# Kernel optimization log

Hardware: AMD Instinct MI355X
Metric: run time of the kernel (lower is better)

The kernel has to match this reference:

```python
import jax, jax.numpy as jnp
import numpy as np

B, T, D, H = 32, 4096, 768, 1024
RHOS = np.linspace(0.1, 0.9, 5)
TAU = 1.0
EPS = 1e-5


def entmax15(x):
    # exact 1.5-entmax along last axis (Peters et al. 2019)
    x = x / 2.0
    x_srt = jnp.flip(jnp.sort(x, axis=-1), axis=-1)  # descending
    n = x.shape[-1]
    rho = jnp.arange(1, n + 1, dtype=x.dtype)
    mean = jnp.cumsum(x_srt, axis=-1) / rho
    mean_sq = jnp.cumsum(x_srt * x_srt, axis=-1) / rho
    ss = rho * (mean_sq - mean * mean)
    delta = (1.0 - ss) / rho
    tau = mean - jnp.sqrt(jnp.clip(delta, 0.0))
    support = jnp.sum(tau <= x_srt, axis=-1, keepdims=True)
    tau_star = jnp.take_along_axis(tau, support - 1, axis=-1)
    return jnp.clip(x - tau_star, 0.0) ** 2


def setup_inputs() -> dict:
    key = jax.random.key(0)
    ks = jax.random.split(key, 8)
    embeddings = jax.random.normal(ks[0], (B, T, D), dtype=jnp.float32)
    ids = jax.random.randint(ks[1], (B, T), 0, 32000)
    lengths = jax.random.randint(ks[2], (B,), T // 4, T + 1)
    attn = (jnp.arange(T)[None, :] < lengths[:, None]).astype(jnp.float32)
    ln_g = jnp.ones((D,), jnp.float32)
    ln_b = jnp.zeros((D,), jnp.float32)
    W1 = 0.02 * jax.random.normal(ks[3], (D, H), dtype=jnp.float32)
    b1 = jnp.zeros((H,), jnp.float32)
    W2 = 0.02 * jax.random.normal(ks[4], (H, 1), dtype=jnp.float32)
    b2 = jnp.zeros((1,), jnp.float32)
    return {"embeddings": embeddings, "attn": attn, "ln_g": ln_g, "ln_b": ln_b,
            "W1": W1, "b1": b1, "W2": W2, "b2": b2, "ids": ids}


def reference(embeddings, attn, ln_g, ln_b, W1, b1, W2, b2, ids):
    emb = embeddings * attn[..., None]                      # [B,T,D]
    mu = jnp.mean(emb, axis=-1, keepdims=True)
    var = jnp.mean((emb - mu) ** 2, axis=-1, keepdims=True)
    xn = (emb - mu) / jnp.sqrt(var + EPS) * ln_g + ln_b
    h1 = jax.nn.gelu(xn @ W1 + b1, approximate=False)       # torch F.gelu (erf)
    scores = (h1 @ W2 + b2)[..., 0]                         # [B,T]
    scores = jnp.where(attn == 0, -1e9, scores)
    z = entmax15(scores / TAU) * attn                       # [B,T]
    sorted_idx = jnp.argsort(-z, axis=-1)                   # descending
    inv_rank = jnp.argsort(sorted_idx, axis=-1)             # rank of each position
    t_eff = jnp.sum(attn, axis=-1)                          # [B]
    rhos = jnp.asarray(RHOS, dtype=z.dtype)                 # [R]
    k = jnp.maximum(1, jnp.floor(rhos[:, None] * t_eff[None, :])).astype(jnp.int32)  # [R,B]
    h = (inv_rank[None] < k[:, :, None]).astype(z.dtype) * attn[None]  # [R,B,T]
    g = jax.lax.stop_gradient(h - z[None]) + z[None]        # straight-through
    return jnp.concatenate([z[None], g], axis=0)            # [1+R, B, T]
```

## Files before the change

### kernel.cpp

```cpp
#include <hip/hip_runtime.h>
#include <math.h>

#define Bc 32
#define Tc 4096
#define Dc 768
#define Hc 1024
#define BTc (Bc*Tc)
#define PLANE 786432

typedef __bf16 bf16x8 __attribute__((ext_vector_type(8)));
typedef float f32x16 __attribute__((ext_vector_type(16)));

__device__ __forceinline__ float gelu_erf(float x) {
  return 0.5f * x * (1.0f + erff(x * 0.70710678118654752440f));
}
__device__ __forceinline__ unsigned bf16rne(float x) {
  unsigned u = __float_as_uint(x);
  return (u + 0x7FFFu + ((u >> 16) & 1u)) >> 16;
}
__device__ __forceinline__ void split3(float x, unsigned& h, unsigned& m, unsigned& l) {
  h = bf16rne(x);
  float r1 = x - __uint_as_float(h << 16);
  m = bf16rne(r1);
  float r2 = r1 - __uint_as_float(m << 16);
  l = bf16rne(r2);
}
__device__ __forceinline__ unsigned f2o(float f) {
  unsigned b = __float_as_uint(f);
  return (b & 0x80000000u) ? ~b : (b | 0x80000000u);
}
__device__ __forceinline__ float o2f(unsigned o) {
  unsigned b = (o & 0x80000000u) ? (o & 0x7FFFFFFFu) : ~o;
  return __uint_as_float(b);
}

struct Bfrag { bf16x8 h[4], m[4], l[4]; };

__device__ __forceinline__ void loadB(const ushort* __restrict__ bp0, Bfrag& B) {
  #pragma unroll
  for (int nt = 0; nt < 4; nt++) {
    const ushort* bp = bp0 + nt * 256;
    B.h[nt] = *(const bf16x8*)(bp);
    B.m[nt] = *(const bf16x8*)(bp + PLANE);
    B.l[nt] = *(const bf16x8*)(bp + 2 * PLANE);
  }
}

__device__ __forceinline__ void mfma6(bf16x8 a0, bf16x8 a1, bf16x8 a2,
                                      const Bfrag& B, f32x16* acc) {
  #pragma unroll
  for (int nt = 0; nt < 4; nt++)
    acc[nt] = __builtin_amdgcn_mfma_f32_32x32x16_bf16(a0, B.h[nt], acc[nt], 0, 0, 0);
  #pragma unroll
  for (int nt = 0; nt < 4; nt++)
    acc[nt] = __builtin_amdgcn_mfma_f32_32x32x16_bf16(a0, B.m[nt], acc[nt], 0, 0, 0);
  #pragma unroll
  for (int nt = 0; nt < 4; nt++)
    acc[nt] = __builtin_amdgcn_mfma_f32_32x32x16_bf16(a1, B.h[nt], acc[nt], 0, 0, 0);
  #pragma unroll
  for (int nt = 0; nt < 4; nt++)
    acc[nt] = __builtin_amdgcn_mfma_f32_32x32x16_bf16(a1, B.m[nt], acc[nt], 0, 0, 0);
  #pragma unroll
  for (int nt = 0; nt < 4; nt++)
    acc[nt] = __builtin_amdgcn_mfma_f32_32x32x16_bf16(a0, B.l[nt], acc[nt], 0, 0, 0);
  #pragma unroll
  for (int nt = 0; nt < 4; nt++)
    acc[nt] = __builtin_amdgcn_mfma_f32_32x32x16_bf16(a2, B.h[nt], acc[nt], 0, 0, 0);
}

__global__ __launch_bounds__(256) void w1_split_k(
    const float* __restrict__ W1, ushort* __restrict__ w1s) {
  int id = blockIdx.x * 256 + threadIdx.x;
  int n = id & 1023, kg = id >> 10;
  unsigned hs[8], ms[8], ls[8];
  #pragma unroll
  for (int j = 0; j < 8; j++) {
    float x = W1[(size_t)(kg * 8 + j) * Hc + n];
    split3(x, hs[j], ms[j], ls[j]);
  }
  size_t o = ((size_t)kg * 1024 + n) * 8;
  int4 ph, pm, pl;
  ph.x = (int)(hs[0] | (hs[1] << 16)); ph.y = (int)(hs[2] | (hs[3] << 16));
  ph.z = (int)(hs[4] | (hs[5] << 16)); ph.w = (int)(hs[6] | (hs[7] << 16));
  pm.x = (int)(ms[0] | (ms[1] << 16)); pm.y = (int)(ms[2] | (ms[3] << 16));
  pm.z = (int)(ms[4] | (ms[5] << 16)); pm.w = (int)(ms[6] | (ms[7] << 16));
  pl.x = (int)(ls[0] | (ls[1] << 16)); pl.y = (int)(ls[2] | (ls[3] << 16));
  pl.z = (int)(ls[4] | (ls[5] << 16)); pl.w = (int)(ls[6] | (ls[7] << 16));
  *(int4*)(w1s + o)             = ph;
  *(int4*)(w1s + o + PLANE)     = pm;
  *(int4*)(w1s + o + 2 * PLANE) = pl;
}

__global__ __launch_bounds__(256) void ln_stats_k(
    const float* __restrict__ emb, const float* __restrict__ attn,
    float* __restrict__ mu, float* __restrict__ rstd) {
  int row = blockIdx.x * 4 + (threadIdx.x >> 6);
  int lane = threadIdx.x & 63;
  float a = attn[row];
  const float4* e = (const float4*)(emb + (size_t)row * Dc);
  float4 v0 = e[lane], v1 = e[lane + 64], v2 = e[lane + 128];
  float x[12] = {v0.x*a, v0.y*a, v0.z*a, v0.w*a,
                 v1.x*a, v1.y*a, v1.z*a, v1.w*a,
                 v2.x*a, v2.y*a, v2.z*a, v2.w*a};
  float s = 0.f;
  #pragma unroll
  for (int i = 0; i < 12; i++) s += x[i];
  #pragma unroll
  for (int o = 32; o; o >>= 1) s += __shfl_xor(s, o);
  float m = s / 768.0f;
  float q = 0.f;
  #pragma unroll
  for (int i = 0; i < 12; i++) { float d = x[i] - m; q += d * d; }
  #pragma unroll
  for (int o = 32; o; o >>= 1) q += __shfl_xor(q, o);
  float var = q / 768.0f;
  if (lane == 0) { mu[row] = m; rstd[row] = 1.0f / sqrtf(var + 1e-5f); }
}

__global__ __launch_bounds__(256, 2) void gemm_scores_mfma8(
    const float* __restrict__ emb, const float* __restrict__ attn,
    const float* __restrict__ ln_g, const float* __restrict__ ln_b,
    const ushort* __restrict__ w1s, const float* __restrict__ b1,
    const float* __restrict__ W2, const float* __restrict__ b2,
    const float* __restrict__ mu, const float* __restrict__ rstd,
    float* __restrict__ spart) {
  __shared__ int4 Abuf[2][3][4][64];
  __shared__ float gls[768], bls[768];
  __shared__ float red[4][64];
  const int id = blockIdx.x;
  const int xcd = id & 7;
  const int y = xcd & 1;
  const int xg = (id >> 3) * 4 + (xcd >> 1);
  const int base = xg * 64;
  if (attn[base] == 0.0f) return;
  const int hbase = y * 512;
  const int t = threadIdx.x;
  const int lane = t & 63;
  const int lrow = lane & 31;
  const int lkg = lane >> 5;
  const int w = t >> 6;

  if (t < 192) {
    *(float4*)&gls[t * 4] = *(const float4*)&ln_g[t * 4];
    *(float4*)&bls[t * 4] = *(const float4*)&ln_b[t * 4];
  }
  const int srow = t & 63;
  const int skg = t >> 6;
  const int skoff = skg * 8;
  const float la  = attn[base + srow];
  const float lmu = mu[base + srow];
  const float lrs = rstd[base + srow];
  const float* erow = emb + (size_t)(base + srow) * Dc + skoff;

  f32x16 acc[8];
  #pragma unroll
  for (int nt = 0; nt < 8; nt++)
    #pragma unroll
    for (int r = 0; r < 16; r++) acc[nt][r] = 0.f;

  __syncthreads();
  {
    float4 e0 = *(const float4*)(erow);
    float4 e1 = *(const float4*)(erow + 4);
    float4 g0 = *(const float4*)&gls[skoff];
    float4 g1 = *(const float4*)&gls[skoff + 4];
    float4 q0 = *(const float4*)&bls[skoff];
    float4 q1 = *(const float4*)&bls[skoff + 4];
    float xs[8] = {e0.x,e0.y,e0.z,e0.w,e1.x,e1.y,e1.z,e1.w};
    float gs[8] = {g0.x,g0.y,g0.z,g0.w,g1.x,g1.y,g1.z,g1.w};
    float bs[8] = {q0.x,q0.y,q0.z,q0.w,q1.x,q1.y,q1.z,q1.w};
    unsigned hh[8], hm[8], hl[8];
    #pragma unroll
    for (int e = 0; e < 8; e++) {
      float xn = (xs[e] * la - lmu) * lrs * gs[e] + bs[e];
      split3(xn, hh[e], hm[e], hl[e]);
    }
    int4 ph, pm, pl;
    ph.x = (int)(hh[0] | (hh[1] << 16)); ph.y = (int)(hh[2] | (hh[3] << 16));
    ph.z = (int)(hh[4] | (hh[5] << 16)); ph.w = (int)(hh[6] | (hh[7] << 16));
    pm.x = (int)(hm[0] | (hm[1] << 16)); pm.y = (int)(hm[2] | (hm[3] << 16));
    pm.z = (int)(hm[4] | (hm[5] << 16)); pm.w = (int)(hm[6] | (hm[7] << 16));
    pl.x = (int)(hl[0] | (hl[1] << 16)); pl.y = (int)(hl[2] | (hl[3] << 16));
    pl.z = (int)(hl[4] | (hl[5] << 16)); pl.w = (int)(hl[6] | (hl[7] << 16));
    Abuf[0][0][skg][srow] = ph;
    Abuf[0][1][skg][srow] = pm;
    Abuf[0][2][skg][srow] = pl;
  }
  __syncthreads();

  const ushort* wbase = w1s + ((size_t)hbase + w * 128 + lrow) * 8;

  #pragma unroll 1
  for (int i = 0; i < 24; i++) {
    const int p = i & 1;
    const bool more = (i < 23);
    #pragma unroll
    for (int kh = 0; kh < 2; kh++) {
      const int kg = kh * 2 + lkg;
      bf16x8 a00 = *(const bf16x8*)&Abuf[p][0][kg][lrow];
      bf16x8 a01 = *(const bf16x8*)&Abuf[p][1][kg][lrow];
      bf16x8 a02 = *(const bf16x8*)&Abuf[p][2][kg][lrow];
      bf16x8 a10 = *(const bf16x8*)&Abuf[p][0][kg][32 + lrow];
      bf16x8 a11 = *(const bf16x8*)&Abuf[p][1][kg][32 + lrow];
      bf16x8 a12 = *(const bf16x8*)&Abuf[p][2][kg][32 + lrow];
      Bfrag B;
      loadB(wbase + (size_t)(i * 4 + kg) * 8192, B);
      mfma6(a00, a01, a02, B, acc);
      mfma6(a10, a11, a12, B, acc + 4);
    }
    if (more) {
      const float* ep = erow + (i + 1) * 32;
      const int koff = (i + 1) * 32 + skoff;
      float4 e0 = *(const float4*)(ep);
      float4 e1 = *(const float4*)(ep + 4);
      float4 g0 = *(const float4*)&gls[koff];
      float4 g1 = *(const float4*)&gls[koff + 4];
      float4 q0 = *(const float4*)&bls[koff];
      float4 q1 = *(const float4*)&bls[koff + 4];
      float xs[8] = {e0.x,e0.y,e0.z,e0.w,e1.x,e1.y,e1.z,e1.w};
      float gs[8] = {g0.x,g0.y,g0.z,g0.w,g1.x,g1.y,g1.z,g1.w};
      float bs[8] = {q0.x,q0.y,q0.z,q0.w,q1.x,q1.y,q1.z,q1.w};
      unsigned hh[8], hm[8], hl[8];
      #pragma unroll
      for (int e = 0; e < 8; e++) {
        float xn = (xs[e] * la - lmu) * lrs * gs[e] + bs[e];
        split3(xn, hh[e], hm[e], hl[e]);
      }
      int4 ph, pm, pl;
      ph.x = (int)(hh[0] | (hh[1] << 16)); ph.y = (int)(hh[2] | (hh[3] << 16));
      ph.z = (int)(hh[4] | (hh[5] << 16)); ph.w = (int)(hh[6] | (hh[7] << 16));
      pm.x = (int)(hm[0] | (hm[1] << 16)); pm.y = (int)(hm[2] | (hm[3] << 16));
      pm.z = (int)(hm[4] | (hm[5] << 16)); pm.w = (int)(hm[6] | (hm[7] << 16));
      pl.x = (int)(hl[0] | (hl[1] << 16)); pl.y = (int)(hl[2] | (hl[3] << 16));
      pl.z = (int)(hl[4] | (hl[5] << 16)); pl.w = (int)(hl[6] | (hl[7] << 16));
      Abuf[p ^ 1][0][skg][srow] = ph;
      Abuf[p ^ 1][1][skg][srow] = pm;
      Abuf[p ^ 1][2][skg][srow] = pl;
    }
    __syncthreads();
  }

  #pragma unroll
  for (int rt = 0; rt < 2; rt++) {
    float sacc[16];
    #pragma unroll
    for (int r = 0; r < 16; r++) sacc[r] = 0.f;
    #pragma unroll
    for (int nt = 0; nt < 4; nt++) {
      const int col = hbase + w * 128 + nt * 32 + lrow;
      const float b1v = b1[col];
      const float w2v = W2[col];
      #pragma unroll
      for (int r = 0; r < 16; r++)
        sacc[r] += gelu_erf(acc[rt * 4 + nt][r] + b1v) * w2v;
    }
    #pragma unroll
    for (int r = 0; r < 16; r++) {
      float v = sacc[r];
      v += __shfl_xor(v, 1);  v += __shfl_xor(v, 2);  v += __shfl_xor(v, 4);
      v += __shfl_xor(v, 8);  v += __shfl_xor(v, 16);
      if (lrow == 0) {
        int row = rt * 32 + (r & 3) + 8 * (r >> 2) + 4 * lkg;
        red[w][row] = v;
      }
    }
  }
  __syncthreads();
  if (t < 64) {
    float v = red[0][t] + red[1][t] + red[2][t] + red[3][t];
    if (y == 0) v += b2[0];
    spart[y * BTc + base + t] = v;
  }
}

__global__ __launch_bounds__(256) void entmax_rank_k(
    const float* __restrict__ sp0, const float* __restrict__ sp1,
    const float* __restrict__ attn, float* __restrict__ out) {
  const int N = 4096;
  __shared__ unsigned long long keys[4096];
  __shared__ double tsum[256], tsq[256];
  __shared__ int tcnt[256];
  __shared__ float sred[4];
  __shared__ double sh_tau;
  __shared__ int sh_S, sh_m, sh_k[5];
  const int b = blockIdx.x;
  const int t = threadIdx.x;
  const float* srow0 = sp0 + b * N;
  const float* srow1 = sp1 + b * N;
  const float* arow = attn + b * N;
  float teff_l = 0.f;
  for (int i = t; i < N; i += 256) {
    float a = arow[i];
    float s = srow0[i] + srow1[i];
    float xe = (a == 0.f) ? -1e9f : s;
    teff_l += a;
    keys[i] = ((unsigned long long)f2o(xe) << 32) |
              (unsigned long long)(0xFFFFFFFFu - (unsigned)i);
  }
  #pragma unroll
  for (int o = 32; o; o >>= 1) teff_l += __shfl_xor(teff_l, o);
  if ((t & 63) == 0) sred[t >> 6] = teff_l;
  __syncthreads();
  if (t == 0) {
    float te = sred[0] + sred[1] + sred[2] + sred[3];
    const float rh[5] = {0.1f, 0.3f, 0.5f, 0.7f, 0.9f};
    for (int r = 0; r < 5; r++) {
      int ki = (int)floorf(rh[r] * te);
      sh_k[r] = ki < 1 ? 1 : ki;
    }
  }
  for (int kk = 2; kk <= N; kk <<= 1) {
    for (int j = kk >> 1; j > 0; j >>= 1) {
      __syncthreads();
      for (int idx = t; idx < N / 2; idx += 256) {
        int i = 2 * idx - (idx & (j - 1));
        int l = i | j;
        unsigned long long A = keys[i], Bv = keys[l];
        bool up = ((i & kk) == 0);
        if (up ? (A < Bv) : (A > Bv)) { keys[i] = Bv; keys[l] = A; }
      }
    }
  }
  __syncthreads();
  const int base = t * 16;
  {
    double ls = 0, lq = 0;
    for (int ii = 0; ii < 16; ii++) {
      double x = 0.5 * (double)o2f((unsigned)(keys[base + ii] >> 32));
      ls += x; lq += x * x;
    }
    tsum[t] = ls; tsq[t] = lq;
  }
  __syncthreads();
  if (t == 0) {
    double rs = 0, rq = 0;
    for (int i = 0; i < 256; i++) {
      double a = tsum[i], c = tsq[i];
      tsum[i] = rs; tsq[i] = rq; rs += a; rq += c;
    }
  }
  __syncthreads();
  {
    double cs = tsum[t], cq = tsq[t];
    int lc = 0;
    for (int ii = 0; ii < 16; ii++) {
      double x = 0.5 * (double)o2f((unsigned)(keys[base + ii] >> 32));
      cs += x; cq += x * x;
      double rho = (double)(base + ii + 1);
      double mean = cs / rho, msq = cq / rho;
      double ss = rho * (msq - mean * mean);
      double delta = (1.0 - ss) / rho;
      double dl = delta > 0.0 ? delta : 0.0;
      double tau = mean - sqrt(dl);
      if (tau <= x) lc++;
    }
    tcnt[t] = lc;
  }
  __syncthreads();
  if (t == 0) {
    int r = 0;
    for (int i = 0; i < 256; i++) { int c = tcnt[i]; tcnt[i] = r; r += c; }
    sh_S = r;
  }
  __syncthreads();
  {
    int jstar = sh_S - 1;
    if (jstar >= base && jstar < base + 16) {
      double cs = tsum[t], cq = tsq[t], tau = 0.0;
      for (int ii = 0; ii <= jstar - base; ii++) {
        double x = 0.5 * (double)o2f((unsigned)(keys[base + ii] >> 32));
        cs += x; cq += x * x;
        double rho = (double)(base + ii + 1);
        double mean = cs / rho, msq = cq / rho;
        double ss = rho * (msq - mean * mean);
        double delta = (1.0 - ss) / rho;
        double dl = delta > 0.0 ? delta : 0.0;
        tau = mean - sqrt(dl);
      }
      sh_tau = tau;
    }
  }
  __syncthreads();
  const double tau = sh_tau;
  float ps[16], pa[16];
  {
    int lf = 0;
    for (int ii = 0; ii < 16; ii++) {
      int p = base + ii;
      ps[ii] = srow0[p] + srow1[p]; pa[ii] = arow[p];
      double d = 0.5 * (double)ps[ii] - tau;
      if (pa[ii] != 0.f && d > 0.0) lf++;
    }
    tcnt[t] = lf;
  }
  __syncthreads();
  if (t == 0) {
    int r = 0;
    for (int i = 0; i < 256; i++) { int c = tcnt[i]; tcnt[i] = r; r += c; }
    sh_m = r;
  }
  __syncthreads();
  const int m = sh_m;
  const int k0_ = sh_k[0], k1_ = sh_k[1], k2_ = sh_k[2], k3_ = sh_k[3], k4_ = sh_k[4];
  {
    int cex = tcnt[t];
    for (int ii = 0; ii < 16; ii++) {
      int p = base + ii;
      double d = 0.5 * (double)ps[ii] - tau;
      bool av = (pa[ii] != 0.f);
      bool sup = av && (d > 0.0);
      out[b * N + p] = sup ? (float)(d * d) : 0.0f;
      if (!sup) {
        int rank = m + p - cex;
        out[1 * BTc + b * N + p] = (av && rank < k0_) ? 1.f : 0.f;
        out[2 * BTc + b * N + p] = (av && rank < k1_) ? 1.f : 0.f;
        out[3 * BTc + b * N + p] = (av && rank < k2_) ? 1.f : 0.f;
        out[4 * BTc + b * N + p] = (av && rank < k3_) ? 1.f : 0.f;
        out[5 * BTc + b * N + p] = (av && rank < k4_) ? 1.f : 0.f;
      } else {
        cex++;
      }
    }
  }
  for (int r = t; r < m; r += 256) {
    int i = (int)(0xFFFFFFFFu - (unsigned)(keys[r] & 0xFFFFFFFFull));
    out[1 * BTc + b * N + i] = (r < k0_) ? 1.f : 0.f;
    out[2 * BTc + b * N + i] = (r < k1_) ? 1.f : 0.f;
    out[3 * BTc + b * N + i] = (r < k2_) ? 1.f : 0.f;
    out[4 * BTc + b * N + i] = (r < k3_) ? 1.f : 0.f;
    out[5 * BTc + b * N + i] = (r < k4_) ? 1.f : 0.f;
  }
}

extern "C" void kernel_launch(void* const* d_in, const int* in_sizes, int n_in,
                              void* d_out, int out_size, void* d_ws, size_t ws_size,
                              hipStream_t stream) {
  (void)in_sizes; (void)n_in; (void)out_size; (void)ws_size;
  const float* emb  = (const float*)d_in[0];
  const float* attn = (const float*)d_in[1];
  const float* ln_g = (const float*)d_in[2];
  const float* ln_b = (const float*)d_in[3];
  const float* W1   = (const float*)d_in[4];
  const float* b1   = (const float*)d_in[5];
  const float* W2   = (const float*)d_in[6];
  const float* b2   = (const float*)d_in[7];
  float* out = (float*)d_out;
  float* wsf = (float*)d_ws;
  float* mu     = wsf;
  float* rstd   = wsf + BTc;
  float* spart  = wsf + 2 * BTc;
  ushort* w1s   = (ushort*)(wsf + 4 * BTc);

  w1_split_k<<<384, 256, 0, stream>>>(W1, w1s);
  ln_stats_k<<<BTc / 4, 256, 0, stream>>>(emb, attn, mu, rstd);
  gemm_scores_mfma8<<<4096, 256, 0, stream>>>(
      emb, attn, ln_g, ln_b, w1s, b1, W2, b2, mu, rstd, spart);
  entmax_rank_k<<<Bc, 256, 0, stream>>>(spart, spart + BTc, attn, out);
}
```

Measured before the change: 980.9 us.

## Stage W1 and embedding tiles into LDS via async global_load_lds double buffering

```diff
diff --git a/kernel.cpp b/kernel.cpp
--- a/kernel.cpp
+++ b/kernel.cpp
@@ -11,6 +11,19 @@
 typedef __bf16 bf16x8 __attribute__((ext_vector_type(8)));
 typedef float f32x16 __attribute__((ext_vector_type(16)));
 
+__device__ __forceinline__ void dma16(const void* g, void* l) {
+  __builtin_amdgcn_global_load_lds(
+      (const __attribute__((address_space(1))) unsigned int*)g,
+      (__attribute__((address_space(3))) unsigned int*)l, 16, 0, 0);
+}
+#define WAITV2() do { asm volatile("s_waitcnt vmcnt(2)" ::: "memory"); \
+                      __builtin_amdgcn_sched_barrier(0); } while (0)
+#define WAITV0() do { asm volatile("s_waitcnt vmcnt(0)" ::: "memory"); \
+                      __builtin_amdgcn_sched_barrier(0); } while (0)
+#define KBARRIER() do { asm volatile("s_waitcnt lgkmcnt(0)" ::: "memory"); \
+                        __builtin_amdgcn_s_barrier(); \
+                        __builtin_amdgcn_sched_barrier(0); } while (0)
+
 __device__ __forceinline__ float gelu_erf(float x) {
   return 0.5f * x * (1.0f + erff(x * 0.70710678118654752440f));
 }
@@ -35,16 +48,6 @@
 }
 
 struct Bfrag { bf16x8 h[4], m[4], l[4]; };
-
-__device__ __forceinline__ void loadB(const ushort* __restrict__ bp0, Bfrag& B) {
-  #pragma unroll
-  for (int nt = 0; nt < 4; nt++) {
-    const ushort* bp = bp0 + nt * 256;
-    B.h[nt] = *(const bf16x8*)(bp);
-    B.m[nt] = *(const bf16x8*)(bp + PLANE);
-    B.l[nt] = *(const bf16x8*)(bp + 2 * PLANE);
-  }
-}
 
 __device__ __forceinline__ void mfma6(bf16x8 a0, bf16x8 a1, bf16x8 a2,
                                       const Bfrag& B, f32x16* acc) {
@@ -117,14 +120,16 @@
   if (lane == 0) { mu[row] = m; rstd[row] = 1.0f / sqrtf(var + 1e-5f); }
 }
 
-__global__ __launch_bounds__(256, 2) void gemm_scores_mfma8(
+__global__ __launch_bounds__(256, 1) void gemm_scores_mfma9(
     const float* __restrict__ emb, const float* __restrict__ attn,
     const float* __restrict__ ln_g, const float* __restrict__ ln_b,
     const ushort* __restrict__ w1s, const float* __restrict__ b1,
     const float* __restrict__ W2, const float* __restrict__ b2,
     const float* __restrict__ mu, const float* __restrict__ rstd,
     float* __restrict__ spart) {
+  __shared__ int4 Bbuf[2][4][12][64];
   __shared__ int4 Abuf[2][3][4][64];
+  __shared__ float Ebuf[2048];
   __shared__ float gls[768], bls[768];
   __shared__ float red[4][64];
   const int id = blockIdx.x;
@@ -144,13 +149,19 @@
     *(float4*)&gls[t * 4] = *(const float4*)&ln_g[t * 4];
     *(float4*)&bls[t * 4] = *(const float4*)&ln_b[t * 4];
   }
-  const int srow = t & 63;
-  const int skg = t >> 6;
-  const int skoff = skg * 8;
+  const int srow = w * 16 + (lane >> 2);
+  const int skc  = lane & 3;
+  const int skoff = skc * 8;
   const float la  = attn[base + srow];
   const float lmu = mu[base + srow];
   const float lrs = rstd[base + srow];
-  const float* erow = emb + (size_t)(base + srow) * Dc + skoff;
+  const int ec0 = srow * 32 + (((skc * 2)    ) ^ (srow & 7)) * 4;
+  const int ec1 = srow * 32 + (((skc * 2) + 1) ^ (srow & 7)) * 4;
+  const int edc = ((lane & 7) ^ ((lane >> 3) & 7)) * 4;
+  const float* esrcA = emb + (size_t)(base + w * 16 + (lane >> 3)) * Dc + edc;
+  const float* esrcB = emb + (size_t)(base + w * 16 + 8 + (lane >> 3)) * Dc + edc;
+  const ushort* bsrc0 = w1s + (size_t)lkg * 8192 +
+                        ((size_t)hbase + w * 128 + lrow) * 8;
 
   f32x16 acc[8];
   #pragma unroll
@@ -160,8 +171,9 @@
 
   __syncthreads();
   {
-    float4 e0 = *(const float4*)(erow);
-    float4 e1 = *(const float4*)(erow + 4);
+    const float* eg = emb + (size_t)(base + srow) * Dc + skoff;
+    float4 e0 = *(const float4*)(eg);
+    float4 e1 = *(const float4*)(eg + 4);
     float4 g0 = *(const float4*)&gls[skoff];
     float4 g1 = *(const float4*)&gls[skoff + 4];
     float4 q0 = *(const float4*)&bls[skoff];
@@ -182,21 +194,40 @@
     pm.z = (int)(hm[4] | (hm[5] << 16)); pm.w = (int)(hm[6] | (hm[7] << 16));
     pl.x = (int)(hl[0] | (hl[1] << 16)); pl.y = (int)(hl[2] | (hl[3] << 16));
     pl.z = (int)(hl[4] | (hl[5] << 16)); pl.w = (int)(hl[6] | (hl[7] << 16));
-    Abuf[0][0][skg][srow] = ph;
-    Abuf[0][1][skg][srow] = pm;
-    Abuf[0][2][skg][srow] = pl;
-  }
-  __syncthreads();
-
-  const ushort* wbase = w1s + ((size_t)hbase + w * 128 + lrow) * 8;
+    Abuf[0][0][skc][srow] = ph;
+    Abuf[0][1][skc][srow] = pm;
+    Abuf[0][2][skc][srow] = pl;
+  }
+  __syncthreads();
+
+  {
+    const ushort* bsp = bsrc0;
+    #pragma unroll
+    for (int s = 0; s < 3; s++)
+      #pragma unroll
+      for (int nt = 0; nt < 4; nt++)
+        dma16(bsp + (size_t)s * PLANE + nt * 256, &Bbuf[0][w][s * 4 + nt][0]);
+  }
 
   #pragma unroll 1
   for (int i = 0; i < 24; i++) {
     const int p = i & 1;
     const bool more = (i < 23);
-    #pragma unroll
-    for (int kh = 0; kh < 2; kh++) {
-      const int kg = kh * 2 + lkg;
+    if (more) {
+      dma16(esrcA + (i + 1) * 32, &Ebuf[w * 512]);
+      dma16(esrcB + (i + 1) * 32, &Ebuf[w * 512 + 256]);
+    }
+    if (more) { WAITV2(); } else { WAITV0(); }
+    {
+      const ushort* bsp = bsrc0 + (size_t)(i * 4 + 2) * 8192;
+      #pragma unroll
+      for (int s = 0; s < 3; s++)
+        #pragma unroll
+        for (int nt = 0; nt < 4; nt++)
+          dma16(bsp + (size_t)s * PLANE + nt * 256, &Bbuf[1][w][s * 4 + nt][0]);
+    }
+    {
+      const int kg = lkg;
       bf16x8 a00 = *(const bf16x8*)&Abuf[p][0][kg][lrow];
       bf16x8 a01 = *(const bf16x8*)&Abuf[p][1][kg][lrow];
       bf16x8 a02 = *(const bf16x8*)&Abuf[p][2][kg][lrow];
@@ -204,20 +235,51 @@
       bf16x8 a11 = *(const bf16x8*)&Abuf[p][1][kg][32 + lrow];
       bf16x8 a12 = *(const bf16x8*)&Abuf[p][2][kg][32 + lrow];
       Bfrag B;
-      loadB(wbase + (size_t)(i * 4 + kg) * 8192, B);
+      #pragma unroll
+      for (int nt = 0; nt < 4; nt++) {
+        B.h[nt] = *(const bf16x8*)&Bbuf[0][w][0 + nt][lane];
+        B.m[nt] = *(const bf16x8*)&Bbuf[0][w][4 + nt][lane];
+        B.l[nt] = *(const bf16x8*)&Bbuf[0][w][8 + nt][lane];
+      }
       mfma6(a00, a01, a02, B, acc);
       mfma6(a10, a11, a12, B, acc + 4);
     }
+    WAITV0();
     if (more) {
-      const float* ep = erow + (i + 1) * 32;
+      const ushort* bsp = bsrc0 + (size_t)((i + 1) * 4) * 8192;
+      #pragma unroll
+      for (int s = 0; s < 3; s++)
+        #pragma unroll
+        for (int nt = 0; nt < 4; nt++)
+          dma16(bsp + (size_t)s * PLANE + nt * 256, &Bbuf[0][w][s * 4 + nt][0]);
+    }
+    {
+      const int kg = 2 + lkg;
+      bf16x8 a00 = *(const bf16x8*)&Abuf[p][0][kg][lrow];
+      bf16x8 a01 = *(const bf16x8*)&Abuf[p][1][kg][lrow];
+      bf16x8 a02 = *(const bf16x8*)&Abuf[p][2][kg][lrow];
+      bf16x8 a10 = *(const bf16x8*)&Abuf[p][0][kg][32 + lrow];
+      bf16x8 a11 = *(const bf16x8*)&Abuf[p][1][kg][32 + lrow];
+      bf16x8 a12 = *(const bf16x8*)&Abuf[p][2][kg][32 + lrow];
+      Bfrag B;
+      #pragma unroll
+      for (int nt = 0; nt < 4; nt++) {
+        B.h[nt] = *(const bf16x8*)&Bbuf[1][w][0 + nt][lane];
+        B.m[nt] = *(const bf16x8*)&Bbuf[1][w][4 + nt][lane];
+        B.l[nt] = *(const bf16x8*)&Bbuf[1][w][8 + nt][lane];
+      }
+      mfma6(a00, a01, a02, B, acc);
+      mfma6(a10, a11, a12, B, acc + 4);
+    }
+    if (more) {
       const int koff = (i + 1) * 32 + skoff;
-      float4 e0 = *(const float4*)(ep);
-      float4 e1 = *(const float4*)(ep + 4);
+      float4 f0 = *(const float4*)&Ebuf[ec0];
+      float4 f1 = *(const float4*)&Ebuf[ec1];
       float4 g0 = *(const float4*)&gls[koff];
       float4 g1 = *(const float4*)&gls[koff + 4];
       float4 q0 = *(const float4*)&bls[koff];
       float4 q1 = *(const float4*)&bls[koff + 4];
-      float xs[8] = {e0.x,e0.y,e0.z,e0.w,e1.x,e1.y,e1.z,e1.w};
+      float xs[8] = {f0.x,f0.y,f0.z,f0.w,f1.x,f1.y,f1.z,f1.w};
       float gs[8] = {g0.x,g0.y,g0.z,g0.w,g1.x,g1.y,g1.z,g1.w};
       float bs[8] = {q0.x,q0.y,q0.z,q0.w,q1.x,q1.y,q1.z,q1.w};
       unsigned hh[8], hm[8], hl[8];
@@ -233,11 +295,11 @@
       pm.z = (int)(hm[4] | (hm[5] << 16)); pm.w = (int)(hm[6] | (hm[7] << 16));
       pl.x = (int)(hl[0] | (hl[1] << 16)); pl.y = (int)(hl[2] | (hl[3] << 16));
       pl.z = (int)(hl[4] | (hl[5] << 16)); pl.w = (int)(hl[6] | (hl[7] << 16));
-      Abuf[p ^ 1][0][skg][srow] = ph;
-      Abuf[p ^ 1][1][skg][srow] = pm;
-      Abuf[p ^ 1][2][skg][srow] = pl;
-    }
-    __syncthreads();
+      Abuf[p ^ 1][0][skc][srow] = ph;
+      Abuf[p ^ 1][1][skc][srow] = pm;
+      Abuf[p ^ 1][2][skc][srow] = pl;
+      KBARRIER();
+    }
   }
 
   #pragma unroll
@@ -453,7 +515,7 @@
 
   w1_split_k<<<384, 256, 0, stream>>>(W1, w1s);
   ln_stats_k<<<BTc / 4, 256, 0, stream>>>(emb, attn, mu, rstd);
-  gemm_scores_mfma8<<<4096, 256, 0, stream>>>(
+  gemm_scores_mfma9<<<4096, 256, 0, stream>>>(
       emb, attn, ln_g, ln_b, w1s, b1, W2, b2, mu, rstd, spart);
   entmax_rank_k<<<Bc, 256, 0, stream>>>(spart, spart + BTc, attn, out);
 }
```

Result: slower. 1.389 ms (+41.6%).

## Enlarge GEMM block tile to 128 rows with 8 waves splitting N

Applied to the files above, without the earlier changes.

```diff
diff --git a/kernel.cpp b/kernel.cpp
--- a/kernel.cpp
+++ b/kernel.cpp
@@ -32,40 +32,6 @@
 __device__ __forceinline__ float o2f(unsigned o) {
   unsigned b = (o & 0x80000000u) ? (o & 0x7FFFFFFFu) : ~o;
   return __uint_as_float(b);
-}
-
-struct Bfrag { bf16x8 h[4], m[4], l[4]; };
-
-__device__ __forceinline__ void loadB(const ushort* __restrict__ bp0, Bfrag& B) {
-  #pragma unroll
-  for (int nt = 0; nt < 4; nt++) {
-    const ushort* bp = bp0 + nt * 256;
-    B.h[nt] = *(const bf16x8*)(bp);
-    B.m[nt] = *(const bf16x8*)(bp + PLANE);
-    B.l[nt] = *(const bf16x8*)(bp + 2 * PLANE);
-  }
-}
-
-__device__ __forceinline__ void mfma6(bf16x8 a0, bf16x8 a1, bf16x8 a2,
-                                      const Bfrag& B, f32x16* acc) {
-  #pragma unroll
-  for (int nt = 0; nt < 4; nt++)
-    acc[nt] = __builtin_amdgcn_mfma_f32_32x32x16_bf16(a0, B.h[nt], acc[nt], 0, 0, 0);
-  #pragma unroll
-  for (int nt = 0; nt < 4; nt++)
-    acc[nt] = __builtin_amdgcn_mfma_f32_32x32x16_bf16(a0, B.m[nt], acc[nt], 0, 0, 0);
-  #pragma unroll
-  for (int nt = 0; nt < 4; nt++)
-    acc[nt] = __builtin_amdgcn_mfma_f32_32x32x16_bf16(a1, B.h[nt], acc[nt], 0, 0, 0);
-  #pragma unroll
-  for (int nt = 0; nt < 4; nt++)
-    acc[nt] = __builtin_amdgcn_mfma_f32_32x32x16_bf16(a1, B.m[nt], acc[nt], 0, 0, 0);
-  #pragma unroll
-  for (int nt = 0; nt < 4; nt++)
-    acc[nt] = __builtin_amdgcn_mfma_f32_32x32x16_bf16(a0, B.l[nt], acc[nt], 0, 0, 0);
-  #pragma unroll
-  for (int nt = 0; nt < 4; nt++)
-    acc[nt] = __builtin_amdgcn_mfma_f32_32x32x16_bf16(a2, B.h[nt], acc[nt], 0, 0, 0);
 }
 
 __global__ __launch_bounds__(256) void w1_split_k(
@@ -117,21 +83,21 @@
   if (lane == 0) { mu[row] = m; rstd[row] = 1.0f / sqrtf(var + 1e-5f); }
 }
 
-__global__ __launch_bounds__(256, 2) void gemm_scores_mfma8(
+__global__ __launch_bounds__(512, 1) void gemm_scores_mfma10(
     const float* __restrict__ emb, const float* __restrict__ attn,
     const float* __restrict__ ln_g, const float* __restrict__ ln_b,
     const ushort* __restrict__ w1s, const float* __restrict__ b1,
     const float* __restrict__ W2, const float* __restrict__ b2,
     const float* __restrict__ mu, const float* __restrict__ rstd,
     float* __restrict__ spart) {
-  __shared__ int4 Abuf[2][3][4][64];
+  __shared__ int4 Abuf[2][3][4][128];
   __shared__ float gls[768], bls[768];
-  __shared__ float red[4][64];
+  __shared__ float red[8][128];
   const int id = blockIdx.x;
   const int xcd = id & 7;
   const int y = xcd & 1;
   const int xg = (id >> 3) * 4 + (xcd >> 1);
-  const int base = xg * 64;
+  const int base = xg * 128;
   if (attn[base] == 0.0f) return;
   const int hbase = y * 512;
   const int t = threadIdx.x;
@@ -144,8 +110,8 @@
     *(float4*)&gls[t * 4] = *(const float4*)&ln_g[t * 4];
     *(float4*)&bls[t * 4] = *(const float4*)&ln_b[t * 4];
   }
-  const int srow = t & 63;
-  const int skg = t >> 6;
+  const int srow = t & 127;
+  const int skg = t >> 7;
   const int skoff = skg * 8;
   const float la  = attn[base + srow];
   const float lmu = mu[base + srow];
@@ -188,7 +154,7 @@
   }
   __syncthreads();
 
-  const ushort* wbase = w1s + ((size_t)hbase + w * 128 + lrow) * 8;
+  const ushort* wbase = w1s + ((size_t)hbase + w * 64 + lrow) * 8;
 
   #pragma unroll 1
   for (int i = 0; i < 24; i++) {
@@ -197,16 +163,32 @@
     #pragma unroll
     for (int kh = 0; kh < 2; kh++) {
       const int kg = kh * 2 + lkg;
-      bf16x8 a00 = *(const bf16x8*)&Abuf[p][0][kg][lrow];
-      bf16x8 a01 = *(const bf16x8*)&Abuf[p][1][kg][lrow];
-      bf16x8 a02 = *(const bf16x8*)&Abuf[p][2][kg][lrow];
-      bf16x8 a10 = *(const bf16x8*)&Abuf[p][0][kg][32 + lrow];
-      bf16x8 a11 = *(const bf16x8*)&Abuf[p][1][kg][32 + lrow];
-      bf16x8 a12 = *(const bf16x8*)&Abuf[p][2][kg][32 + lrow];
-      Bfrag B;
-      loadB(wbase + (size_t)(i * 4 + kg) * 8192, B);
-      mfma6(a00, a01, a02, B, acc);
-      mfma6(a10, a11, a12, B, acc + 4);
+      const ushort* bp = wbase + (size_t)(i * 4 + kg) * 8192;
+      bf16x8 Bh0 = *(const bf16x8*)(bp);
+      bf16x8 Bh1 = *(const bf16x8*)(bp + 256);
+      bf16x8 Bm0 = *(const bf16x8*)(bp + PLANE);
+      bf16x8 Bm1 = *(const bf16x8*)(bp + PLANE + 256);
+      bf16x8 Bl0 = *(const bf16x8*)(bp + 2 * PLANE);
+      bf16x8 Bl1 = *(const bf16x8*)(bp + 2 * PLANE + 256);
+      #pragma unroll
+      for (int rt = 0; rt < 4; rt++) {
+        bf16x8 a0 = *(const bf16x8*)&Abuf[p][0][kg][rt * 32 + lrow];
+        bf16x8 a1 = *(const bf16x8*)&Abuf[p][1][kg][rt * 32 + lrow];
+        bf16x8 a2 = *(const bf16x8*)&Abuf[p][2][kg][rt * 32 + lrow];
+        f32x16* ac = acc + rt * 2;
+        ac[0] = __builtin_amdgcn_mfma_f32_32x32x16_bf16(a0, Bh0, ac[0], 0, 0, 0);
+        ac[1] = __builtin_amdgcn_mfma_f32_32x32x16_bf16(a0, Bh1, ac[1], 0, 0, 0);
+        ac[0] = __builtin_amdgcn_mfma_f32_32x32x16_bf16(a0, Bm0, ac[0], 0, 0, 0);
+        ac[1] = __builtin_amdgcn_mfma_f32_32x32x16_bf16(a0, Bm1, ac[1], 0, 0, 0);
+        ac[0] = __builtin_amdgcn_mfma_f32_32x32x16_bf16(a1, Bh0, ac[0], 0, 0, 0);
+        ac[1] = __builtin_amdgcn_mfma_f32_32x32x16_bf16(a1, Bh1, ac[1], 0, 0, 0);
+        ac[0] = __builtin_amdgcn_mfma_f32_32x32x16_bf16(a1, Bm0, ac[0], 0, 0, 0);
+        ac[1] = __builtin_amdgcn_mfma_f32_32x32x16_bf16(a1, Bm1, ac[1], 0, 0, 0);
+        ac[0] = __builtin_amdgcn_mfma_f32_32x32x16_bf16(a0, Bl0, ac[0], 0, 0, 0);
+        ac[1] = __builtin_amdgcn_mfma_f32_32x32x16_bf16(a0, Bl1, ac[1], 0, 0, 0);
+        ac[0] = __builtin_amdgcn_mfma_f32_32x32x16_bf16(a2, Bh0, ac[0], 0, 0, 0);
+        ac[1] = __builtin_amdgcn_mfma_f32_32x32x16_bf16(a2, Bh1, ac[1], 0, 0, 0);
+      }
     }
     if (more) {
       const float* ep = erow + (i + 1) * 32;
@@ -241,18 +223,18 @@
   }
 
   #pragma unroll
-  for (int rt = 0; rt < 2; rt++) {
+  for (int rt = 0; rt < 4; rt++) {
     float sacc[16];
     #pragma unroll
     for (int r = 0; r < 16; r++) sacc[r] = 0.f;
     #pragma unroll
-    for (int nt = 0; nt < 4; nt++) {
-      const int col = hbase + w * 128 + nt * 32 + lrow;
+    for (int nt = 0; nt < 2; nt++) {
+      const int col = hbase + w * 64 + nt * 32 + lrow;
       const float b1v = b1[col];
       const float w2v = W2[col];
       #pragma unroll
       for (int r = 0; r < 16; r++)
-        sacc[r] += gelu_erf(acc[rt * 4 + nt][r] + b1v) * w2v;
+        sacc[r] += gelu_erf(acc[rt * 2 + nt][r] + b1v) * w2v;
     }
     #pragma unroll
     for (int r = 0; r < 16; r++) {
@@ -266,8 +248,9 @@
     }
   }
   __syncthreads();
-  if (t < 64) {
-    float v = red[0][t] + red[1][t] + red[2][t] + red[3][t];
+  if (t < 128) {
+    float v = red[0][t] + red[1][t] + red[2][t] + red[3][t] +
+              red[4][t] + red[5][t] + red[6][t] + red[7][t];
     if (y == 0) v += b2[0];
     spart[y * BTc + base + t] = v;
   }
@@ -453,7 +436,7 @@
 
   w1_split_k<<<384, 256, 0, stream>>>(W1, w1s);
   ln_stats_k<<<BTc / 4, 256, 0, stream>>>(emb, attn, mu, rstd);
-  gemm_scores_mfma8<<<4096, 256, 0, stream>>>(
+  gemm_scores_mfma10<<<2048, 512, 0, stream>>>(
       emb, attn, ln_g, ln_b, w1s, b1, W2, b2, mu, rstd, spart);
   entmax_rank_k<<<Bc, 256, 0, stream>>>(spart, spart + BTc, attn, out);
 }
```

After: 1.100 ms. 12.1% more time.
